# Performance work log

Hardware: AMD Instinct MI355X
Metric: run time of the kernel (lower is better)

Reference implementation:

```python
import jax, jax.numpy as jnp
import numpy as np
from math import ceil

RATIO = 0.5
NUM_GRAPHS = 512
NODES_PER_GRAPH = 1024
N = NUM_GRAPHS * NODES_PER_GRAPH
C = 64
E = 16 * N


def setup_inputs() -> dict:
    key = jax.random.key(0)
    k1, k2 = jax.random.split(key)
    x = jax.random.normal(k1, (N, C), dtype=jnp.float32)
    edge_index = jax.random.randint(k2, (2, E), 0, N, dtype=jnp.int64)
    batch = jnp.repeat(jnp.arange(NUM_GRAPHS, dtype=jnp.int64), NODES_PER_GRAPH)
    return {"x": x, "edge_index": edge_index, "batch": batch,
            "num_graphs": NUM_GRAPHS, "max_num_nodes": NODES_PER_GRAPH}


def reference(x, edge_index, batch, num_graphs, max_num_nodes):
    n = max_num_nodes
    k_sel = ceil(n * RATIO)
    num_nodes = x.shape[0]
    # per-graph: sorted random subset of k_sel local node ids, offset by graph block
    keys = jax.random.split(jax.random.key(42), num_graphs)
    local = jax.vmap(lambda k: jnp.sort(jax.random.permutation(k, n)[:k_sel]))(keys)  # [B, k_sel]
    offsets = jnp.arange(num_graphs, dtype=local.dtype)[:, None] * n
    perm = (local + offsets).reshape(-1)  # [B*k_sel] global node ids, sorted within each graph

    x_sel = x[perm]
    batch_sel = batch[perm]

    # filter_adj: relabel kept nodes 0..K-1, drop edges touching removed nodes
    idx_dtype = edge_index.dtype
    mask = jnp.full((num_nodes,), -1, dtype=idx_dtype)
    mask = mask.at[perm].set(jnp.arange(perm.shape[0], dtype=idx_dtype))
    row = mask[edge_index[0]]
    col = mask[edge_index[1]]
    keep = (row >= 0) & (col >= 0)
    # fixed-shape variant of the dynamic filter: dropped edges marked -1
    new_edge_index = jnp.where(keep[None, :], jnp.stack([row, col]), -1)
    return (x_sel, new_edge_index, batch_sel, perm)
```

## Files before the change

kernel.cpp:

```cpp
#include <hip/hip_runtime.h>

#define NUM_GRAPHS 512
#define NPG        1024
#define KSEL       512
#define NNODES     (NUM_GRAPHS * NPG)
#define CFEAT      64
#define NEDGE      (16 * NNODES)
#define NWORDS     (NUM_GRAPHS * 32)

typedef int   int4v   __attribute__((ext_vector_type(4)));
typedef float float4v __attribute__((ext_vector_type(4)));

__device__ __forceinline__ unsigned rotl32(unsigned v, int d) {
  return (v << d) | (v >> (32 - d));
}

__device__ __forceinline__ void tf2x32(unsigned k0, unsigned k1,
                                       unsigned x0, unsigned x1,
                                       unsigned& o0, unsigned& o1) {
  unsigned ks2 = k0 ^ k1 ^ 0x1BD11BDAu;
  x0 += k0; x1 += k1;
  x0 += x1; x1 = rotl32(x1, 13); x1 ^= x0;
  x0 += x1; x1 = rotl32(x1, 15); x1 ^= x0;
  x0 += x1; x1 = rotl32(x1, 26); x1 ^= x0;
  x0 += x1; x1 = rotl32(x1, 6);  x1 ^= x0;
  x0 += k1; x1 += ks2 + 1u;
  x0 += x1; x1 = rotl32(x1, 17); x1 ^= x0;
  x0 += x1; x1 = rotl32(x1, 29); x1 ^= x0;
  x0 += x1; x1 = rotl32(x1, 16); x1 ^= x0;
  x0 += x1; x1 = rotl32(x1, 24); x1 ^= x0;
  x0 += ks2; x1 += k0 + 2u;
  x0 += x1; x1 = rotl32(x1, 13); x1 ^= x0;
  x0 += x1; x1 = rotl32(x1, 15); x1 ^= x0;
  x0 += x1; x1 = rotl32(x1, 26); x1 ^= x0;
  x0 += x1; x1 = rotl32(x1, 6);  x1 ^= x0;
  x0 += k0; x1 += k1 + 3u;
  x0 += x1; x1 = rotl32(x1, 17); x1 ^= x0;
  x0 += x1; x1 = rotl32(x1, 29); x1 ^= x0;
  x0 += x1; x1 = rotl32(x1, 16); x1 ^= x0;
  x0 += x1; x1 = rotl32(x1, 24); x1 ^= x0;
  x0 += k1; x1 += ks2 + 4u;
  x0 += x1; x1 = rotl32(x1, 13); x1 ^= x0;
  x0 += x1; x1 = rotl32(x1, 15); x1 ^= x0;
  x0 += x1; x1 = rotl32(x1, 26); x1 ^= x0;
  x0 += x1; x1 = rotl32(x1, 6);  x1 ^= x0;
  x0 += ks2; x1 += k0 + 5u;
  o0 = x0; o1 = x1;
}

__global__ __launch_bounds__(512) void tab_kernel(
    float* __restrict__ out_b, float* __restrict__ out_p,
    unsigned long long* __restrict__ tab,
    unsigned short* __restrict__ ids_ws) {
  __shared__ int bins[256];
  __shared__ unsigned long long cand[NPG];
  __shared__ unsigned long long words64[16];
  __shared__ int wbase[16];
  __shared__ int ccnt;
  __shared__ int sB, sR;
  __shared__ unsigned long long sT;

  const int g = blockIdx.x;
  const int tid = threadIdx.x;
  const int lane = tid & 63;
  const int wv = tid >> 6;

  unsigned kg0, kg1, sk0, sk1;
  tf2x32(0u, 42u, 0u, (unsigned)g, kg0, kg1);
  tf2x32(kg0, kg1, 0u, 1u, sk0, sk1);

  if (tid < 256) bins[tid] = 0;
  if (tid == 0) ccnt = 0;

  unsigned long long myk[2];
#pragma unroll
  for (int e = 0; e < 2; ++e) {
    int i = e * 512 + tid;
    unsigned b1, b2;
    tf2x32(sk0, sk1, 0u, (unsigned)i, b1, b2);
    unsigned key = b1 ^ b2;
    myk[e] = ((unsigned long long)key << 32) | (unsigned)i;
  }
  __syncthreads();

#pragma unroll
  for (int e = 0; e < 2; ++e)
    atomicAdd(&bins[(int)(myk[e] >> 56)], 1);
  __syncthreads();

  if (tid < 64) {
    int b0 = bins[4 * tid], b1 = bins[4 * tid + 1],
        b2 = bins[4 * tid + 2], b3 = bins[4 * tid + 3];
    int s = b0 + b1 + b2 + b3;
    int inc = s;
#pragma unroll
    for (int d = 1; d < 64; d <<= 1) {
      int t = __shfl_up(inc, d, 64);
      if (tid >= d) inc += t;
    }
    int excl = inc - s;
    int i0 = excl + b0, i1 = i0 + b1, i2 = i1 + b2, i3 = i2 + b3;
    if (excl < KSEL && KSEL <= i0) { sB = 4 * tid;     sR = KSEL - excl; }
    if (i0   < KSEL && KSEL <= i1) { sB = 4 * tid + 1; sR = KSEL - i0; }
    if (i1   < KSEL && KSEL <= i2) { sB = 4 * tid + 2; sR = KSEL - i1; }
    if (i2   < KSEL && KSEL <= i3) { sB = 4 * tid + 3; sR = KSEL - i2; }
  }
  __syncthreads();
  const int bstar = sB;
  const int r = sR;

#pragma unroll
  for (int e = 0; e < 2; ++e) {
    if ((int)(myk[e] >> 56) == bstar) {
      int p = atomicAdd(&ccnt, 1);
      cand[p] = myk[e];
    }
  }
  __syncthreads();
  const int cnt = ccnt;
  if (tid < 64) {
    for (int c = tid; c < cnt; c += 64) {
      unsigned long long mine = cand[c];
      int rank = 0;
      for (int j = 0; j < cnt; ++j) rank += (cand[j] < mine) ? 1 : 0;
      if (rank == r - 1) sT = mine;
    }
  }
  __syncthreads();
  const unsigned long long T = sT;

  const bool sel0 = (myk[0] <= T);
  const bool sel1 = (myk[1] <= T);
  {
    unsigned long long b0 = __ballot(sel0);
    unsigned long long b1 = __ballot(sel1);
    if (lane == 0) {
      words64[wv] = b0;
      words64[8 + wv] = b1;
    }
  }
  __syncthreads();

  if (tid < 16) {
    int c = __popcll(words64[tid]);
    int inc = c;
#pragma unroll
    for (int d = 1; d < 16; d <<= 1) {
      int t = __shfl_up(inc, d, 64);
      if (tid >= d) inc += t;
    }
    wbase[tid] = inc - c;
  }
  __syncthreads();

#pragma unroll
  for (int e = 0; e < 2; ++e) {
    bool sel = e ? sel1 : sel0;
    if (sel) {
      int i = e * 512 + tid;
      int wi = i >> 6;
      int l = i & 63;
      unsigned long long w = words64[wi];
      int pos = wbase[wi] + __popcll(w & ((1ull << l) - 1ull));
      ids_ws[g * KSEL + pos] = (unsigned short)i;
      out_b[g * KSEL + pos] = (float)g;
      out_p[g * KSEL + pos] = (float)(g * NPG + i);
    }
  }

  if (tid < 32) {
    unsigned long long w64 = words64[tid >> 1];
    unsigned w32 = (unsigned)(w64 >> ((tid & 1) * 32));
    unsigned base = (unsigned)wbase[tid >> 1] +
                    ((tid & 1) ? (unsigned)__popc((unsigned)w64) : 0u);
    tab[g * 32 + tid] = (unsigned long long)w32 |
                        ((unsigned long long)base << 32);
  }
}

__global__ __launch_bounds__(1024) void fused_kernel(
    const float* __restrict__ x, const int* __restrict__ ei,
    const unsigned long long* __restrict__ tab,
    const unsigned short* __restrict__ ids_ws,
    float* __restrict__ out_x, float* __restrict__ out_e) {
  __shared__ unsigned long long ltab[NWORDS];
  __shared__ unsigned short lids[1024];

  const int tid = threadIdx.x;
  const int blk = blockIdx.x;

#pragma unroll
  for (int k = 0; k < NWORDS / 1024; ++k) {
    ltab[k * 1024 + tid] = tab[k * 1024 + tid];
  }
  {
    const int row0 = blk * 1024;
    if (tid < 512) {
      ((unsigned*)lids)[tid] = ((const unsigned*)(ids_ws + row0))[tid];
    }
  }
  __syncthreads();

  {
    const float4v* xs = (const float4v*)x;
    float4v* xd = (float4v*)out_x;
    const int row0 = blk * 1024;
#pragma unroll
    for (int k = 0; k < 16; ++k) {
      int t = k * 1024 + tid;
      int r = t >> 4;
      int c = t & 15;
      int row = row0 + r;
      int g = row >> 9;
      int id = lids[r];
      float4v v = __builtin_nontemporal_load(
          &xs[((size_t)g * NPG + id) * 16 + c]);
      __builtin_nontemporal_store(v, &xd[(size_t)row * 16 + c]);
    }
  }

#pragma unroll
  for (int k = 0; k < 4; ++k) {
    const int base = (((k * 256 + blk) * 1024) + tid) * 8;
    int4v s0 = __builtin_nontemporal_load((const int4v*)(ei + base));
    int4v s1 = __builtin_nontemporal_load((const int4v*)(ei + base + 4));
    int4v d0 = __builtin_nontemporal_load((const int4v*)(ei + (size_t)NEDGE + base));
    int4v d1 = __builtin_nontemporal_load((const int4v*)(ei + (size_t)NEDGE + base + 4));

    int src[8] = {s0.x, s0.y, s0.z, s0.w, s1.x, s1.y, s1.z, s1.w};
    int dst[8] = {d0.x, d0.y, d0.z, d0.w, d1.x, d1.y, d1.z, d1.w};

    int rrow[8], rcol[8];
#pragma unroll
    for (int j = 0; j < 8; ++j) {
      unsigned long long es = ltab[src[j] >> 5];
      unsigned long long ed = ltab[dst[j] >> 5];
      unsigned ws = (unsigned)es, wd = (unsigned)ed;
      int shs = src[j] & 31, shd = dst[j] & 31;
      bool sels = (ws >> shs) & 1u;
      bool seld = (wd >> shd) & 1u;
      int poss = (int)(es >> 32) + __popc(ws & ((1u << shs) - 1u));
      int posd = (int)(ed >> 32) + __popc(wd & ((1u << shd) - 1u));
      bool keep = sels && seld;
      rrow[j] = keep ? (((src[j] & ~1023) >> 1) + poss) : -1;
      rcol[j] = keep ? (((dst[j] & ~1023) >> 1) + posd) : -1;
    }

    float4v r0 = {(float)rrow[0], (float)rrow[1], (float)rrow[2], (float)rrow[3]};
    float4v r1 = {(float)rrow[4], (float)rrow[5], (float)rrow[6], (float)rrow[7]};
    float4v c0 = {(float)rcol[0], (float)rcol[1], (float)rcol[2], (float)rcol[3]};
    float4v c1 = {(float)rcol[4], (float)rcol[5], (float)rcol[6], (float)rcol[7]};
    __builtin_nontemporal_store(r0, (float4v*)(out_e + base));
    __builtin_nontemporal_store(r1, (float4v*)(out_e + base + 4));
    __builtin_nontemporal_store(c0, (float4v*)(out_e + (size_t)NEDGE + base));
    __builtin_nontemporal_store(c1, (float4v*)(out_e + (size_t)NEDGE + base + 4));
  }
}

extern "C" void kernel_launch(void* const* d_in, const int* in_sizes, int n_in,
                              void* d_out, int out_size, void* d_ws, size_t ws_size,
                              hipStream_t stream) {
  const float* x  = (const float*)d_in[0];
  const int*   ei = (const int*)d_in[1];

  float* out   = (float*)d_out;
  float* out_x = out;
  float* out_e = out + (size_t)NUM_GRAPHS * KSEL * CFEAT;
  float* out_b = out_e + 2 * (size_t)NEDGE;
  float* out_p = out_b + (size_t)NUM_GRAPHS * KSEL;

  unsigned long long* tab = (unsigned long long*)d_ws;
  unsigned short* ids_ws = (unsigned short*)((char*)d_ws + NWORDS * 8);

  tab_kernel<<<NUM_GRAPHS, 512, 0, stream>>>(out_b, out_p, tab, ids_ws);
  fused_kernel<<<256, 1024, 0, stream>>>(x, ei, tab, ids_ws, out_x, out_e);
}
```

Measured before the change: 279.7 us.

## Move feature gather into selection kernel using shared-memory ids

Moves the x row gather from the edge kernel into the per-graph selection kernel, which now keeps the selected local ids in shared memory instead of writing them to a workspace. The edge kernel only filters and relabels edges. This drops the ids workspace round trip and gives the selection kernel memory work to overlap with its compute. The cost is that the gather now runs in the smaller 512-thread selection grid and is no longer overlapped with the edge traffic in one kernel.

```diff
diff --git a/kernel.cpp b/kernel.cpp
--- a/kernel.cpp
+++ b/kernel.cpp
@@ -48,14 +48,15 @@
   o0 = x0; o1 = x1;
 }
 
-__global__ __launch_bounds__(512) void tab_kernel(
+__global__ __launch_bounds__(512) void select_kernel(
+    const float* __restrict__ x, float* __restrict__ out_x,
     float* __restrict__ out_b, float* __restrict__ out_p,
-    unsigned long long* __restrict__ tab,
-    unsigned short* __restrict__ ids_ws) {
+    unsigned long long* __restrict__ tab) {
   __shared__ int bins[256];
   __shared__ unsigned long long cand[NPG];
   __shared__ unsigned long long words64[16];
   __shared__ int wbase[16];
+  __shared__ short ids[KSEL];
   __shared__ int ccnt;
   __shared__ int sB, sR;
   __shared__ unsigned long long sT;
@@ -162,7 +163,7 @@
       int l = i & 63;
       unsigned long long w = words64[wi];
       int pos = wbase[wi] + __popcll(w & ((1ull << l) - 1ull));
-      ids_ws[g * KSEL + pos] = (unsigned short)i;
+      ids[pos] = (short)i;
       out_b[g * KSEL + pos] = (float)g;
       out_p[g * KSEL + pos] = (float)(g * NPG + i);
     }
@@ -176,15 +177,28 @@
     tab[g * 32 + tid] = (unsigned long long)w32 |
                         ((unsigned long long)base << 32);
   }
-}
-
-__global__ __launch_bounds__(1024) void fused_kernel(
-    const float* __restrict__ x, const int* __restrict__ ei,
+  __syncthreads();
+
+  {
+    const float4v* xs = (const float4v*)x + (size_t)g * (NPG * 16);
+    float4v* xd = (float4v*)out_x + (size_t)g * (KSEL * 16);
+#pragma unroll
+    for (int k = 0; k < 16; ++k) {
+      int t = k * 512 + tid;
+      int rr = t >> 4;
+      int c = t & 15;
+      int id = (int)ids[rr];
+      float4v v = __builtin_nontemporal_load(&xs[id * 16 + c]);
+      __builtin_nontemporal_store(v, &xd[rr * 16 + c]);
+    }
+  }
+}
+
+__global__ __launch_bounds__(1024) void edge_kernel(
+    const int* __restrict__ ei,
     const unsigned long long* __restrict__ tab,
-    const unsigned short* __restrict__ ids_ws,
-    float* __restrict__ out_x, float* __restrict__ out_e) {
+    float* __restrict__ out_e) {
   __shared__ unsigned long long ltab[NWORDS];
-  __shared__ unsigned short lids[1024];
 
   const int tid = threadIdx.x;
   const int blk = blockIdx.x;
@@ -193,31 +207,7 @@
   for (int k = 0; k < NWORDS / 1024; ++k) {
     ltab[k * 1024 + tid] = tab[k * 1024 + tid];
   }
-  {
-    const int row0 = blk * 1024;
-    if (tid < 512) {
-      ((unsigned*)lids)[tid] = ((const unsigned*)(ids_ws + row0))[tid];
-    }
-  }
-  __syncthreads();
-
-  {
-    const float4v* xs = (const float4v*)x;
-    float4v* xd = (float4v*)out_x;
-    const int row0 = blk * 1024;
-#pragma unroll
-    for (int k = 0; k < 16; ++k) {
-      int t = k * 1024 + tid;
-      int r = t >> 4;
-      int c = t & 15;
-      int row = row0 + r;
-      int g = row >> 9;
-      int id = lids[r];
-      float4v v = __builtin_nontemporal_load(
-          &xs[((size_t)g * NPG + id) * 16 + c]);
-      __builtin_nontemporal_store(v, &xd[(size_t)row * 16 + c]);
-    }
-  }
+  __syncthreads();
 
 #pragma unroll
   for (int k = 0; k < 4; ++k) {
@@ -270,8 +260,7 @@
   float* out_p = out_b + (size_t)NUM_GRAPHS * KSEL;
 
   unsigned long long* tab = (unsigned long long*)d_ws;
-  unsigned short* ids_ws = (unsigned short*)((char*)d_ws + NWORDS * 8);
-
-  tab_kernel<<<NUM_GRAPHS, 512, 0, stream>>>(out_b, out_p, tab, ids_ws);
-  fused_kernel<<<256, 1024, 0, stream>>>(x, ei, tab, ids_ws, out_x, out_e);
-}
+
+  select_kernel<<<NUM_GRAPHS, 512, 0, stream>>>(x, out_x, out_b, out_p, tab);
+  edge_kernel<<<256, 1024, 0, stream>>>(ei, tab, out_e);
+}
```

Result: no change. 276.5 us (-1.1%).
